# Optimization experiments

Measured on AMD Instinct MI355X. Metric: run time of the kernel, lower is better.

Reference implementation:

```python
import jax, jax.numpy as jnp
import numpy as np
from jax import lax

# dims: batch, item seq len, d_model, d_inner, d_state, d_conv, dt_rank, n_layers
B, L, H, E, N, K, R, NL = 256, 200, 256, 512, 16, 4, 16, 2
V = 150000            # int(n_items * 1.5)
USER_ID = 1
T = L + L // 2        # interleaved length
EPS = 1e-12

FLOATS = ('item_emb', 'ln_w', 'ln_b', 'in_proj_w', 'conv_w', 'conv_b', 'x_proj_w',
          'dt_w', 'dt_b', 'A_log', 'Dp', 'out_w', 'mn_w', 'mn_b',
          'fc1_w', 'fc1_b', 'fc2_w', 'fc2_b', 'fn_w', 'fn_b')


def setup_inputs():
    key = jax.random.key(0)
    ks = jax.random.split(key, 12)
    g = lambda k, s: jax.random.normal(k, s, jnp.float32) * 0.02
    return dict(
        item_seq=jax.random.randint(ks[0], (B, L), 0, 100000),
        seq_len=jax.random.randint(ks[1], (B,), 0, 200),
        item_emb=g(ks[2], (V, H)),
        ln_w=jnp.ones((H,)), ln_b=jnp.zeros((H,)),
        in_proj_w=g(ks[3], (NL, 2 * E, H)),
        conv_w=g(ks[4], (NL, E, K)), conv_b=jnp.zeros((NL, E)),
        x_proj_w=g(ks[5], (NL, R + 2 * N, E)),
        dt_w=g(ks[6], (NL, E, R)), dt_b=jnp.zeros((NL, E)),
        A_log=jnp.tile(jnp.log(jnp.arange(1, N + 1, dtype=jnp.float32)), (NL, E, 1)),
        Dp=jnp.ones((NL, E)),
        out_w=g(ks[7], (NL, H, E)),
        mn_w=jnp.ones((NL, H)), mn_b=jnp.zeros((NL, H)),
        fc1_w=g(ks[8], (NL, 4 * H, H)), fc1_b=jnp.zeros((NL, 4 * H)),
        fc2_w=g(ks[9], (NL, H, 4 * H)), fc2_b=jnp.zeros((NL, H)),
        fn_w=jnp.ones((NL, H)), fn_b=jnp.zeros((NL, H)),
    )


def _ln(x, w, b):
    m = x.mean(-1, keepdims=True)
    v = x.var(-1, keepdims=True)
    return (x - m) * lax.rsqrt(v + EPS) * w + b


def _interleave(seq):
    # [B,L] -> [B, L + L//2], user separator after every 2 items
    i = jnp.arange(L)
    out = jnp.zeros((seq.shape[0], T), seq.dtype)
    out = out.at[:, i + i // 2].set(seq)
    io = jnp.arange(1, L, 2)            # odd positions close a pair
    out = out.at[:, io + io // 2 + 1].set(-USER_ID)
    return out


def _selective_scan(xc, dt, Bm, Cm, A, D):
    # xc, dt: [B,T,E]; Bm, Cm: [B,T,N]; A: [E,N]; D: [E]
    def step(s, ins):
        x_t, dt_t, b_t, c_t = ins                     # [B,E],[B,E],[B,N],[B,N]
        s = s * jnp.exp(dt_t[..., None] * A) + (dt_t * x_t)[..., None] * b_t[:, None, :]
        return s, jnp.einsum('ben,bn->be', s, c_t)
    s0 = jnp.zeros((xc.shape[0], E, N), xc.dtype)
    xs = tuple(a.swapaxes(0, 1) for a in (xc, dt, Bm, Cm))
    _, ys = lax.scan(step, s0, xs)
    return ys.swapaxes(0, 1) + xc * D


def _mamba(x, p):
    xz = x @ p['in_proj_w'].T                         # [B,T,2E]
    xc, z = jnp.split(xz, 2, axis=-1)
    xcT = lax.conv_general_dilated(xc.swapaxes(1, 2), p['conv_w'][:, None, :], (1,),
                                   [(K - 1, 0)], dimension_numbers=('NCH', 'OIH', 'NCH'),
                                   feature_group_count=E)
    xc = jax.nn.silu(xcT + p['conv_b'][None, :, None]).swapaxes(1, 2)  # causal depthwise conv
    xdbl = xc @ p['x_proj_w'].T                       # [B,T,R+2N]
    dt = jax.nn.softplus(xdbl[..., :R] @ p['dt_w'].T + p['dt_b'])
    Bm, Cm = xdbl[..., R:R + N], xdbl[..., R + N:]
    y = _selective_scan(xc, dt, Bm, Cm, -jnp.exp(p['A_log']), p['Dp'])
    return (y * jax.nn.silu(z)) @ p['out_w'].T


def _core(item_seq, seq_len, F):
    tot = _interleave(item_seq)
    tot = jnp.where(tot < 0, tot + V, tot)            # negative user id wraps into table
    h = _ln(F['item_emb'][tot], F['ln_w'], F['ln_b'])  # dropout is identity (eval)
    per = ('in_proj_w', 'conv_w', 'conv_b', 'x_proj_w', 'dt_w', 'dt_b', 'A_log', 'Dp', 'out_w')
    for l in range(NL):
        p = {k: F[k][l] for k in per}
        h = _ln(_mamba(h, p) + h, F['mn_w'][l], F['mn_b'][l])   # use_residual=True (NL>1)
        ff = jax.nn.gelu(h @ F['fc1_w'][l].T + F['fc1_b'][l], approximate=False)
        ff = ff @ F['fc2_w'][l].T + F['fc2_b'][l]
        h = _ln(ff + h, F['fn_w'][l], F['fn_b'][l])
    tl = seq_len + seq_len // 2
    idx = jnp.clip(tl - 1, 0, T - 1)
    return h[jnp.arange(h.shape[0]), idx]             # gather last valid position


def reference(item_seq, seq_len, item_emb, ln_w, ln_b, in_proj_w, conv_w, conv_b,
              x_proj_w, dt_w, dt_b, A_log, Dp, out_w, mn_w, mn_b,
              fc1_w, fc1_b, fc2_w, fc2_b, fn_w, fn_b):
    F = dict(zip(FLOATS, (item_emb, ln_w, ln_b, in_proj_w, conv_w, conv_b, x_proj_w,
                          dt_w, dt_b, A_log, Dp, out_w, mn_w, mn_b,
                          fc1_w, fc1_b, fc2_w, fc2_b, fn_w, fn_b)))
    return _core(item_seq, seq_len, F)
```

## Files before the change

kernel.cpp:

```cpp
#include <hip/hip_runtime.h>
#include <math.h>

typedef unsigned short u16;
typedef __attribute__((ext_vector_type(8))) short bf8_t;
typedef __attribute__((ext_vector_type(4))) float f4_t;

#define BB 256
#define LL 200
#define HH 256
#define EE 512
#define NSTATE 16
#define KCONV 4
#define RR 16
#define NLAYER 2
#define VV 150000
#define TT 300
#define MTOK (BB*TT)
#define NC 6
#define CL 50
#define XW 1024

#define LOG2E 1.44269504088896340736f
#define LN2   0.69314718055994530942f

__device__ __forceinline__ float geluf(float x) {
    return 0.5f * x * (1.0f + erff(x * 0.70710678118654752440f));
}
__device__ __forceinline__ u16 f2bf(float x) {
    unsigned u = __float_as_uint(x);
    unsigned r = u + 0x7FFF + ((u >> 16) & 1);
    return (u16)(r >> 16);
}
__device__ __forceinline__ float bf2f(u16 b) { return __uint_as_float((unsigned)b << 16); }

__device__ __forceinline__ void gload16(const void* gp, void* lp) {
    __builtin_amdgcn_global_load_lds(
        (const __attribute__((address_space(1))) unsigned int*)gp,
        (__attribute__((address_space(3))) unsigned int*)lp,
        16, 0, 0);
}

__device__ __forceinline__ void block_reduce2(float& a, float& b) {
    __shared__ float ra[4], rb[4];
    #pragma unroll
    for (int o = 32; o > 0; o >>= 1) {
        a += __shfl_down(a, o, 64);
        b += __shfl_down(b, o, 64);
    }
    int lane = threadIdx.x & 63, w = threadIdx.x >> 6;
    if (lane == 0) { ra[w] = a; rb[w] = b; }
    __syncthreads();
    a = ra[0] + ra[1] + ra[2] + ra[3];
    b = rb[0] + rb[1] + rb[2] + rb[3];
}

__global__ __launch_bounds__(256)
void split_kernel(const float* __restrict__ x, u16* __restrict__ ph,
                  u16* __restrict__ pl, int n) {
    int i = blockIdx.x * 256 + threadIdx.x;
    if (i < n) {
        float v = x[i];
        u16 hb = f2bf(v);
        ph[i] = hb;
        pl[i] = f2bf(v - bf2f(hb));
    }
}

__global__ __launch_bounds__(256)
void embed_ln_kernel(const int* __restrict__ item_seq,
                     const float* __restrict__ item_emb,
                     const float* __restrict__ ln_w,
                     const float* __restrict__ ln_b,
                     u16* __restrict__ hh, u16* __restrict__ hl) {
    int tok = blockIdx.x;
    int b = tok / TT, p = tok - b * TT;
    int k = p / 3, r = p - 3 * k;
    int item;
    if (r == 2) item = VV - 1;
    else        item = item_seq[b * LL + 2 * k + r];
    int tid = threadIdx.x;
    float x = item_emb[(size_t)item * HH + tid];
    float s1 = x, s2 = x * x;
    block_reduce2(s1, s2);
    float m = s1 * (1.0f / HH);
    float var = s2 * (1.0f / HH) - m * m;
    float inv = rsqrtf(var + 1e-12f);
    float v = (x - m) * inv * ln_w[tid] + ln_b[tid];
    size_t idx = (size_t)tok * HH + tid;
    u16 hb = f2bf(v);
    hh[idx] = hb;
    hl[idx] = f2bf(v - bf2f(hb));
}

__global__ __launch_bounds__(256)
void add_ln_kernel(const float* __restrict__ tmp,
                   u16* __restrict__ hh, u16* __restrict__ hl,
                   const float* __restrict__ w,
                   const float* __restrict__ bnorm) {
    int tok = blockIdx.x;
    int tid = threadIdx.x;
    size_t idx = (size_t)tok * HH + tid;
    float x = tmp[idx] + bf2f(hh[idx]) + bf2f(hl[idx]);
    float s1 = x, s2 = x * x;
    block_reduce2(s1, s2);
    float m = s1 * (1.0f / HH);
    float var = s2 * (1.0f / HH) - m * m;
    float inv = rsqrtf(var + 1e-12f);
    float v = (x - m) * inv * w[tid] + bnorm[tid];
    u16 hb = f2bf(v);
    hh[idx] = hb;
    hl[idx] = f2bf(v - bf2f(hb));
}

template <int AMODE, int MODE>
__global__ __launch_bounds__(256)
void gemm_mfma(const u16* __restrict__ Ah, const u16* __restrict__ Al, int ldab,
               const u16* __restrict__ Wh,
               const float* __restrict__ bias,
               float* __restrict__ C, u16* __restrict__ Cb,
               int M, int N, int K, int ldc) {
    __shared__ u16 sA[2][2][128 * 32];
    __shared__ u16 sB[2][128 * 32];
    int tid = threadIdx.x;
    int lane = tid & 63, wid = tid >> 6;
    int wr = wid >> 1, wc = wid & 1;

    int gx = gridDim.x, nwg = gx * gridDim.y;
    int id = blockIdx.y * gx + blockIdx.x;
    int q = nwg >> 3, rr8 = nwg & 7;
    int xcd = id & 7, pos = id >> 3;
    int nid = (xcd < rr8 ? xcd * (q + 1) : rr8 * (q + 1) + (xcd - rr8) * q) + pos;
    int bn = (nid % gx) * 128;
    int bm = (nid / gx) * 128;

    f4_t acc[4][4];
    #pragma unroll
    for (int i = 0; i < 4; ++i)
        #pragma unroll
        for (int j = 0; j < 4; ++j)
            acc[i][j] = (f4_t){0.f, 0.f, 0.f, 0.f};

    int scol = (lane & 3) * 8;

    auto stageA = [&](int bi, int k0) {
        #pragma unroll
        for (int qq = 0; qq < 2; ++qq) {
            int row = wid * 32 + qq * 16 + (lane >> 2);
            size_t ga = (size_t)(bm + row) * ldab + k0 + scol;
            int off = (wid * 2 + qq) * 1024;
            gload16(Ah + ga, (char*)&sA[bi][0][0] + off);
            if (AMODE == 0)
                gload16(Al + ga, (char*)&sA[bi][1][0] + off);
        }
    };
    auto stageB = [&](int bi, int k0) {
        #pragma unroll
        for (int qq = 0; qq < 2; ++qq) {
            int row = wid * 32 + qq * 16 + (lane >> 2);
            size_t gb = (size_t)(bn + row) * K + k0 + scol;
            int off = (wid * 2 + qq) * 1024;
            gload16(Wh + gb, (char*)&sB[bi][0] + off);
        }
    };
    auto compute = [&](int bi) {
        int arow = wr * 64 + (lane & 15);
        int koff = (lane >> 4) * 8;
        bf8_t ah[4], al[4];
        #pragma unroll
        for (int fm = 0; fm < 4; ++fm) {
            int r = arow + fm * 16;
            ah[fm] = *(const bf8_t*)&sA[bi][0][r * 32 + koff];
            if (AMODE == 0)
                al[fm] = *(const bf8_t*)&sA[bi][1][r * 32 + koff];
        }
        #pragma unroll
        for (int fn = 0; fn < 4; ++fn) {
            int r = wc * 64 + fn * 16 + (lane & 15);
            bf8_t bh = *(const bf8_t*)&sB[bi][r * 32 + koff];
            #pragma unroll
            for (int fm = 0; fm < 4; ++fm) {
                acc[fm][fn] = __builtin_amdgcn_mfma_f32_16x16x32_bf16(ah[fm], bh, acc[fm][fn], 0, 0, 0);
                if (AMODE == 0)
                    acc[fm][fn] = __builtin_amdgcn_mfma_f32_16x16x32_bf16(al[fm], bh, acc[fm][fn], 0, 0, 0);
            }
        }
    };

    stageA(0, 0);
    stageB(0, 0);
    __syncthreads();
    int cur = 0;
    for (int k0 = 0; k0 < K; k0 += 32) {
        if (k0 + 32 < K) {
            stageA(cur ^ 1, k0 + 32);
            stageB(cur ^ 1, k0 + 32);
        }
        compute(cur);
        __syncthreads();
        cur ^= 1;
    }

    if (MODE == 2 || MODE == 3) {
        u16* rs = (u16*)&sA[0][0][0];
        #pragma unroll
        for (int fn = 0; fn < 4; ++fn) {
            int cl = wc * 64 + fn * 16 + (lane & 15);
            float bv = (bias != nullptr) ? bias[bn + cl] : 0.f;
            #pragma unroll
            for (int fm = 0; fm < 4; ++fm) {
                #pragma unroll
                for (int j = 0; j < 4; ++j) {
                    int lr = wr * 64 + fm * 16 + (lane >> 4) * 4 + j;
                    float v = acc[fm][fn][j] + bv;
                    if (MODE == 2) v = geluf(v);
                    rs[lr * 128 + cl] = f2bf(v);
                }
            }
        }
        __syncthreads();
        int r = tid >> 1, half = tid & 1;
        u16* dst = Cb + (size_t)(bm + r) * ldc + bn + half * 64;
        const u16* src = rs + r * 128 + half * 64;
        #pragma unroll
        for (int i = 0; i < 8; ++i)
            *(bf8_t*)&dst[i * 8] = *(const bf8_t*)&src[i * 8];
    } else {
        #pragma unroll
        for (int fn = 0; fn < 4; ++fn) {
            int colg = bn + wc * 64 + fn * 16 + (lane & 15);
            if (colg < N) {
                float bv = (bias != nullptr) ? bias[colg] : 0.f;
                #pragma unroll
                for (int fm = 0; fm < 4; ++fm) {
                    #pragma unroll
                    for (int j = 0; j < 4; ++j) {
                        int rowg = bm + wr * 64 + fm * 16 + (lane >> 4) * 4 + j;
                        C[(size_t)rowg * ldc + colg] = acc[fm][fn][j] + bv;
                    }
                }
            }
        }
    }
}

__global__ __launch_bounds__(256)
void gemm_xproj(const u16* __restrict__ Axz,
                const u16* __restrict__ Wh, const u16* __restrict__ Wl,
                float* __restrict__ C) {
    __shared__ u16 sA[2][128 * 32];
    __shared__ u16 sB[2][2][48 * 32];
    int tid = threadIdx.x;
    int lane = tid & 63, wid = tid >> 6;
    int bm = blockIdx.x * 128;

    f4_t acc[2][3];
    #pragma unroll
    for (int i = 0; i < 2; ++i)
        #pragma unroll
        for (int j = 0; j < 3; ++j)
            acc[i][j] = (f4_t){0.f, 0.f, 0.f, 0.f};

    int scol = (lane & 3) * 8;

    auto stage = [&](int bi, int k0) {
        #pragma unroll
        for (int qq = 0; qq < 2; ++qq) {
            int row = wid * 32 + qq * 16 + (lane >> 2);
            size_t ga = (size_t)(bm + row) * XW + k0 + scol;
            int off = (wid * 2 + qq) * 1024;
            gload16(Axz + ga, (char*)&sA[bi][0] + off);
        }
        if (tid < 192) {
            int row = tid >> 2;
            int c16 = (tid & 3) * 8;
            size_t gb = (size_t)row * EE + k0 + c16;
            gload16(Wh + gb, (char*)&sB[bi][0][0] + tid * 16);
            gload16(Wl + gb, (char*)&sB[bi][1][0] + tid * 16);
        }
    };
    auto compute = [&](int bi) {
        int arow = wid * 32 + (lane & 15);
        int koff = (lane >> 4) * 8;
        bf8_t ah[2];
        #pragma unroll
        for (int fm = 0; fm < 2; ++fm) {
            int r = arow + fm * 16;
            ah[fm] = *(const bf8_t*)&sA[bi][r * 32 + koff];
        }
        #pragma unroll
        for (int fn = 0; fn < 3; ++fn) {
            int r = fn * 16 + (lane & 15);
            bf8_t bh = *(const bf8_t*)&sB[bi][0][r * 32 + koff];
            bf8_t bl = *(const bf8_t*)&sB[bi][1][r * 32 + koff];
            #pragma unroll
            for (int fm = 0; fm < 2; ++fm) {
                acc[fm][fn] = __builtin_amdgcn_mfma_f32_16x16x32_bf16(ah[fm], bh, acc[fm][fn], 0, 0, 0);
                acc[fm][fn] = __builtin_amdgcn_mfma_f32_16x16x32_bf16(ah[fm], bl, acc[fm][fn], 0, 0, 0);
            }
        }
    };

    stage(0, 0);
    __syncthreads();
    int cur = 0;
    for (int k0 = 0; k0 < EE; k0 += 32) {
        if (k0 + 32 < EE) stage(cur ^ 1, k0 + 32);
        compute(cur);
        __syncthreads();
        cur ^= 1;
    }

    #pragma unroll
    for (int fn = 0; fn < 3; ++fn) {
        int colg = fn * 16 + (lane & 15);
        #pragma unroll
        for (int fm = 0; fm < 2; ++fm) {
            #pragma unroll
            for (int j = 0; j < 4; ++j) {
                int rowg = bm + wid * 32 + fm * 16 + (lane >> 4) * 4 + j;
                C[(size_t)rowg * 48 + colg] = acc[fm][fn][j];
            }
        }
    }
}

__global__ __launch_bounds__(256)
void conv_halo_kernel(const u16* __restrict__ xzb, float* __restrict__ halo) {
    int bid = blockIdx.x;
    int ehalf = bid & 1, bc = bid >> 1;
    int c = bc % NC, b = bc / NC;
    int e = ehalf * 256 + threadIdx.x;
    int t0 = c * CL;
    const u16* xp = xzb + (size_t)b * TT * XW + e;
    float* hp = halo + (((size_t)b * NC + c) * 3) * EE + e;
    #pragma unroll
    for (int k = 0; k < 3; ++k) {
        int t = t0 - 3 + k;
        hp[(size_t)k * EE] = (t >= 0) ? bf2f(xp[(size_t)t * XW]) : 0.f;
    }
}

__global__ __launch_bounds__(256)
void conv_chunk_kernel(u16* __restrict__ xzb, const float* __restrict__ halo,
                       const float* __restrict__ conv_w,
                       const float* __restrict__ conv_b, int layer) {
    int bid = blockIdx.x;
    int ehalf = bid & 1, bc = bid >> 1;
    int c = bc % NC, b = bc / NC;
    int e = ehalf * 256 + threadIdx.x;
    int t0 = c * CL;
    const float* w = conv_w + ((size_t)layer * EE + e) * KCONV;
    float w0 = w[0], w1 = w[1], w2 = w[2], w3 = w[3];
    float bias = conv_b[layer * EE + e];
    const float* hp = halo + (((size_t)b * NC + c) * 3) * EE + e;
    float h0 = hp[0], h1 = hp[(size_t)EE], h2 = hp[(size_t)2 * EE];
    u16* p = xzb + ((size_t)b * TT + t0) * XW + e;

    float c0 = bf2f(p[0]);
    float c1 = bf2f(p[(size_t)XW]);
    for (int tg = 0; tg < CL; tg += 2) {
        float n0, n1;
        if (tg + 2 < CL) {
            n0 = bf2f(p[(size_t)(tg + 2) * XW]);
            n1 = bf2f(p[(size_t)(tg + 3) * XW]);
        }
        float v0 = fmaf(w0, h0, fmaf(w1, h1, fmaf(w2, h2, fmaf(w3, c0, bias))));
        float v1 = fmaf(w0, h1, fmaf(w1, h2, fmaf(w2, c0, fmaf(w3, c1, bias))));
        p[(size_t)(tg + 0) * XW] = f2bf(v0 / (1.f + __expf(-v0)));
        p[(size_t)(tg + 1) * XW] = f2bf(v1 / (1.f + __expf(-v1)));
        h0 = h2; h1 = c0; h2 = c1;
        if (tg + 2 < CL) { c0 = n0; c1 = n1; }
    }
}

template <bool CHAIN, bool EMIT>
__device__ __forceinline__ void scan_chunk_body(
        const float* __restrict__ rowp,
        u16* __restrict__ xp,
        const float* __restrict__ dw, float db,
        const float* __restrict__ arl2e,
        float Dv, float2* __restrict__ s2, float& dsum) {
    float xc0 = bf2f(xp[0]), xc1 = bf2f(xp[(size_t)XW]);
    float zc0, zc1;
    if (EMIT) { zc0 = bf2f(xp[EE]); zc1 = bf2f(xp[(size_t)XW + EE]); }
    for (int tg = 0; tg < CL; tg += 2) {
        float xn0, xn1, zn0, zn1;
        if (tg + 2 < CL) {
            xn0 = bf2f(xp[(size_t)(tg + 2) * XW]);
            xn1 = bf2f(xp[(size_t)(tg + 3) * XW]);
            if (EMIT) {
                zn0 = bf2f(xp[(size_t)(tg + 2) * XW + EE]);
                zn1 = bf2f(xp[(size_t)(tg + 3) * XW + EE]);
            }
        }
        #pragma unroll
        for (int i = 0; i < 2; ++i) {
            int t = tg + i;
            const float* row = rowp + (size_t)t * 48;
            float2 racc = make_float2(db, 0.f);
            #pragma unroll
            for (int j = 0; j < 16; j += 2) {
                float2 rv = *(const float2*)(row + j);
                float2 wv = *(const float2*)(dw + j);
                racc += rv * wv;
            }
            float rr = racc.x + racc.y;
            float qv = exp2f(-fabsf(rr) * LOG2E);
            float dt = fmaxf(rr, 0.f) + LN2 * __log2f(1.f + qv);
            if (!EMIT) dsum += dt;
            float xv = (i == 0) ? xc0 : xc1;
            float dx = dt * xv;
            float2 P[8];
            if (CHAIN) {
                float w1 = exp2f(dt * arl2e[0]);
                float w2 = w1 * w1;
                float2 w2v = make_float2(w2, w2);
                P[0] = make_float2(w1, w2);
                #pragma unroll
                for (int k = 1; k < 8; ++k) P[k] = P[k - 1] * w2v;
            } else {
                #pragma unroll
                for (int k = 0; k < 8; ++k)
                    P[k] = make_float2(exp2f(dt * arl2e[2 * k]),
                                       exp2f(dt * arl2e[2 * k + 1]));
            }
            float2 dx2 = make_float2(dx, dx);
            float2 qa = make_float2(0.f, 0.f), qb = make_float2(0.f, 0.f);
            #pragma unroll
            for (int k = 0; k < 8; ++k) {
                float2 Bv = *(const float2*)(row + 16 + 2 * k);
                s2[k] = s2[k] * P[k] + dx2 * Bv;
                if (EMIT) {
                    float2 Cv = *(const float2*)(row + 32 + 2 * k);
                    if (k & 1) qb += s2[k] * Cv;
                    else       qa += s2[k] * Cv;
                }
            }
            if (EMIT) {
                float2 qs = qa + qb;
                float y = (qs.x + qs.y) + xv * Dv;
                float zv = (i == 0) ? zc0 : zc1;
                float u = y * (zv / (1.f + __expf(-zv)));
                xp[(size_t)t * XW] = f2bf(u);
            }
        }
        if (tg + 2 < CL) {
            xc0 = xn0; xc1 = xn1;
            if (EMIT) { zc0 = zn0; zc1 = zn1; }
        }
    }
}

__device__ __forceinline__ void load_scan_params(
        const float* dt_w, const float* dt_b, const float* A_log,
        int layer, int e, float* dw, float& db, float* arl2e, bool& chain) {
    #pragma unroll
    for (int i = 0; i < 16; i += 4)
        *(float4*)&dw[i] = *(const float4*)(dt_w + ((size_t)layer * EE + e) * RR + i);
    db = dt_b[layer * EE + e];
    const float* alp = A_log + ((size_t)layer * EE + e) * NSTATE;
    float ar[16];
    #pragma unroll
    for (int i = 0; i < 16; i += 4) {
        float4 v = *(const float4*)(alp + i);
        ar[i + 0] = -expf(v.x); ar[i + 1] = -expf(v.y);
        ar[i + 2] = -expf(v.z); ar[i + 3] = -expf(v.w);
    }
    chain = true;
    #pragma unroll
    for (int n = 1; n < 16; ++n)
        chain = chain && (fabsf(ar[n] - (n + 1) * ar[0]) <= 1e-3f * (n + 1) * fabsf(ar[0]));
    #pragma unroll
    for (int n = 0; n < 16; ++n) arl2e[n] = ar[n] * LOG2E;
}

__global__ __launch_bounds__(256, 1)
void scan_p1(const float* __restrict__ xdbl, u16* __restrict__ xzb,
             const float* __restrict__ dt_w, const float* __restrict__ dt_b,
             const float* __restrict__ A_log,
             float* __restrict__ SF, float* __restrict__ DS, int layer) {
    int bid = blockIdx.x;
    int ehalf = bid & 1, bc = bid >> 1;
    int c = bc % NC, b = bc / NC;
    int e = ehalf * 256 + threadIdx.x;
    int t0 = c * CL;
    alignas(16) float dw[16], arl2e[16];
    float db; bool chain;
    load_scan_params(dt_w, dt_b, A_log, layer, e, dw, db, arl2e, chain);

    const float* rowp = xdbl + ((size_t)b * TT + t0) * 48;
    u16* xp = xzb + ((size_t)b * TT + t0) * XW + e;
    float2 s2[8];
    #pragma unroll
    for (int k = 0; k < 8; ++k) s2[k] = make_float2(0.f, 0.f);
    float dsum = 0.f;
    if (chain) scan_chunk_body<true, false>(rowp, xp, dw, db, arl2e, 0.f, s2, dsum);
    else       scan_chunk_body<false, false>(rowp, xp, dw, db, arl2e, 0.f, s2, dsum);
    size_t sbase = (((size_t)b * EE + e) * NC + c) * 16;
    #pragma unroll
    for (int k = 0; k < 8; ++k) *(float2*)(SF + sbase + 2 * k) = s2[k];
    DS[((size_t)b * EE + e) * NC + c] = dsum;
}

__global__ __launch_bounds__(256)
void scan_p2(const float* __restrict__ A_log,
             float* __restrict__ SF, const float* __restrict__ DS, int layer) {
    int g = blockIdx.x * 256 + threadIdx.x;
    int e = g & (EE - 1), b = g >> 9;
    const float* alp = A_log + ((size_t)layer * EE + e) * NSTATE;
    float arl2e[16];
    #pragma unroll
    for (int i = 0; i < 16; i += 4) {
        float4 v = *(const float4*)(alp + i);
        arl2e[i + 0] = -expf(v.x) * LOG2E; arl2e[i + 1] = -expf(v.y) * LOG2E;
        arl2e[i + 2] = -expf(v.z) * LOG2E; arl2e[i + 3] = -expf(v.w) * LOG2E;
    }
    float s[16];
    #pragma unroll
    for (int n = 0; n < 16; ++n) s[n] = 0.f;
    size_t base = ((size_t)b * EE + e) * NC;
    for (int c = 0; c < NC; ++c) {
        float ds = DS[base + c];
        alignas(16) float f[16];
        #pragma unroll
        for (int i = 0; i < 16; i += 4) *(float4*)&f[i] = *(const float4*)(SF + (base + c) * 16 + i);
        #pragma unroll
        for (int i = 0; i < 16; i += 4) *(float4*)(SF + (base + c) * 16 + i) = *(float4*)&s[i];
        #pragma unroll
        for (int n = 0; n < 16; ++n) s[n] = fmaf(s[n], exp2f(ds * arl2e[n]), f[n]);
    }
}

__global__ __launch_bounds__(256, 1)
void scan_p3(const float* __restrict__ xdbl, u16* __restrict__ xzb,
             const float* __restrict__ dt_w, const float* __restrict__ dt_b,
             const float* __restrict__ A_log, const float* __restrict__ Dp,
             const float* __restrict__ SF, int layer) {
    int bid = blockIdx.x;
    int ehalf = bid & 1, bc = bid >> 1;
    int c = bc % NC, b = bc / NC;
    int e = ehalf * 256 + threadIdx.x;
    int t0 = c * CL;
    alignas(16) float dw[16], arl2e[16];
    float db; bool chain;
    load_scan_params(dt_w, dt_b, A_log, layer, e, dw, db, arl2e, chain);
    float Dv = Dp[layer * EE + e];

    const float* rowp = xdbl + ((size_t)b * TT + t0) * 48;
    u16* xp = xzb + ((size_t)b * TT + t0) * XW + e;
    float2 s2[8];
    size_t sbase = (((size_t)b * EE + e) * NC + c) * 16;
    #pragma unroll
    for (int k = 0; k < 8; ++k) s2[k] = *(const float2*)(SF + sbase + 2 * k);
    float dsum = 0.f;
    if (chain) scan_chunk_body<true, true>(rowp, xp, dw, db, arl2e, Dv, s2, dsum);
    else       scan_chunk_body<false, true>(rowp, xp, dw, db, arl2e, Dv, s2, dsum);
}

__global__ __launch_bounds__(256)
void gather_out_kernel(const u16* __restrict__ hh, const u16* __restrict__ hl,
                       const int* __restrict__ seq_len,
                       float* __restrict__ out) {
    int b = blockIdx.x;
    int sl = seq_len[b];
    int tl = sl + sl / 2;
    int idx = tl - 1;
    if (idx < 0) idx = 0;
    if (idx > TT - 1) idx = TT - 1;
    size_t src = ((size_t)b * TT + idx) * HH + threadIdx.x;
    out[(size_t)b * HH + threadIdx.x] = bf2f(hh[src]) + bf2f(hl[src]);
}

extern "C" void kernel_launch(void* const* d_in, const int* in_sizes, int n_in,
                              void* d_out, int out_size, void* d_ws, size_t ws_size,
                              hipStream_t stream) {
    const int*   item_seq  = (const int*)  d_in[0];
    const int*   seq_len   = (const int*)  d_in[1];
    const float* item_emb  = (const float*)d_in[2];
    const float* ln_w      = (const float*)d_in[3];
    const float* ln_b      = (const float*)d_in[4];
    const float* in_proj_w = (const float*)d_in[5];
    const float* conv_w    = (const float*)d_in[6];
    const float* conv_b    = (const float*)d_in[7];
    const float* x_proj_w  = (const float*)d_in[8];
    const float* dt_w      = (const float*)d_in[9];
    const float* dt_b      = (const float*)d_in[10];
    const float* A_log     = (const float*)d_in[11];
    const float* Dp        = (const float*)d_in[12];
    const float* out_w     = (const float*)d_in[13];
    const float* mn_w      = (const float*)d_in[14];
    const float* mn_b      = (const float*)d_in[15];
    const float* fc1_w     = (const float*)d_in[16];
    const float* fc1_b     = (const float*)d_in[17];
    const float* fc2_w     = (const float*)d_in[18];
    const float* fc2_b     = (const float*)d_in[19];
    const float* fn_w      = (const float*)d_in[20];
    const float* fn_b      = (const float*)d_in[21];

    u16*   xzb  = (u16*)d_ws;
    u16*   hh   = xzb + (size_t)MTOK * XW;
    u16*   hl   = hh + (size_t)MTOK * HH;
    float* tmp  = (float*)(hl + (size_t)MTOK * HH);
    float* xdbl = tmp;
    float* SF   = tmp + (size_t)3686400;
    float* DS   = tmp + (size_t)16269312;
    float* halo = tmp + (size_t)17055744;
    u16* pw   = (u16*)(tmp + (size_t)MTOK * HH);
    u16* inH  = pw;                 u16* inL  = inH  + 524288;
    u16* xpH  = inL  + 524288;      u16* xpL  = xpH  + 49152;
    u16* outH = xpL  + 49152;       u16* outL = outH + 262144;
    u16* f1H  = outL + 262144;      u16* f1L  = f1H  + 524288;
    u16* f2H  = f1L  + 524288;      u16* f2L  = f2H  + 524288;
    u16* ffb = xzb;

    split_kernel<<<524288 / 256, 256, 0, stream>>>(in_proj_w, inH, inL, 524288);
    split_kernel<<<49152 / 256, 256, 0, stream>>>(x_proj_w, xpH, xpL, 49152);
    split_kernel<<<262144 / 256, 256, 0, stream>>>(out_w, outH, outL, 262144);
    split_kernel<<<524288 / 256, 256, 0, stream>>>(fc1_w, f1H, f1L, 524288);
    split_kernel<<<524288 / 256, 256, 0, stream>>>(fc2_w, f2H, f2L, 524288);

    embed_ln_kernel<<<MTOK, 256, 0, stream>>>(item_seq, item_emb, ln_w, ln_b, hh, hl);

    const int gscan = BB * NC * 2;

    for (int l = 0; l < NLAYER; ++l) {
        {
            dim3 grid((2 * EE) / 128, MTOK / 128);
            gemm_mfma<0, 3><<<grid, 256, 0, stream>>>(
                hh, hl, HH,
                inH + (size_t)l * 262144,
                nullptr, nullptr, xzb, MTOK, 2 * EE, HH, XW);
        }
        conv_halo_kernel<<<gscan, 256, 0, stream>>>(xzb, halo);
        conv_chunk_kernel<<<gscan, 256, 0, stream>>>(xzb, halo, conv_w, conv_b, l);
        gemm_xproj<<<MTOK / 128, 256, 0, stream>>>(
            xzb, xpH + (size_t)l * 24576, xpL + (size_t)l * 24576, xdbl);
        scan_p1<<<gscan, 256, 0, stream>>>(xdbl, xzb, dt_w, dt_b, A_log, SF, DS, l);
        scan_p2<<<(BB * EE) / 256, 256, 0, stream>>>(A_log, SF, DS, l);
        scan_p3<<<gscan, 256, 0, stream>>>(xdbl, xzb, dt_w, dt_b, A_log, Dp, SF, l);
        {
            dim3 grid(HH / 128, MTOK / 128);
            gemm_mfma<3, 0><<<grid, 256, 0, stream>>>(
                xzb, nullptr, XW,
                outH + (size_t)l * 131072,
                nullptr, tmp, nullptr, MTOK, HH, EE, HH);
        }
        add_ln_kernel<<<MTOK, 256, 0, stream>>>(tmp, hh, hl, mn_w + l * HH, mn_b + l * HH);
        {
            dim3 grid((4 * HH) / 128, MTOK / 128);
            gemm_mfma<0, 2><<<grid, 256, 0, stream>>>(
                hh, hl, HH,
                f1H + (size_t)l * 262144,
                fc1_b + (size_t)l * 4 * HH,
                nullptr, ffb, MTOK, 4 * HH, HH, XW);
        }
        {
            dim3 grid(HH / 128, MTOK / 128);
            gemm_mfma<3, 0><<<grid, 256, 0, stream>>>(
                ffb, nullptr, XW,
                f2H + (size_t)l * 262144,
                fc2_b + (size_t)l * HH,
                tmp, nullptr, MTOK, HH, 4 * HH, HH);
        }
        add_ln_kernel<<<MTOK, 256, 0, stream>>>(tmp, hh, hl, fn_w + l * HH, fn_b + l * HH);
    }

    gather_out_kernel<<<BB, 256, 0, stream>>>(hh, hl, seq_len, (float*)d_out);
}
```

Before: 1.735 ms.

## Drop low-part activation MFMA in GEMMs and scan two channels per thread

The in_proj and fc1 GEMMs no longer load or multiply the low bf16 residual of the activations, so each uses half the MFMAs and A-tile traffic, at some cost in accuracy. Separately, the scan phase kernels now handle two adjacent channels per thread, with 32-bit packed x/z loads and stores and shared B/C/dt-row loads. This halves the scan grid and raises per-thread register pressure. The chain check is factored into a helper, and the full A vector is loaded only on the non-chain path.

```diff
diff --git a/kernel.cpp b/kernel.cpp
--- a/kernel.cpp
+++ b/kernel.cpp
@@ -112,14 +112,14 @@
     hl[idx] = f2bf(v - bf2f(hb));
 }
 
-template <int AMODE, int MODE>
-__global__ __launch_bounds__(256)
-void gemm_mfma(const u16* __restrict__ Ah, const u16* __restrict__ Al, int ldab,
+template <int MODE>
+__global__ __launch_bounds__(256)
+void gemm_mfma(const u16* __restrict__ Ah, int ldab,
                const u16* __restrict__ Wh,
                const float* __restrict__ bias,
                float* __restrict__ C, u16* __restrict__ Cb,
                int M, int N, int K, int ldc) {
-    __shared__ u16 sA[2][2][128 * 32];
+    __shared__ u16 sA[2][128 * 32];
     __shared__ u16 sB[2][128 * 32];
     int tid = threadIdx.x;
     int lane = tid & 63, wid = tid >> 6;
@@ -148,9 +148,7 @@
             int row = wid * 32 + qq * 16 + (lane >> 2);
             size_t ga = (size_t)(bm + row) * ldab + k0 + scol;
             int off = (wid * 2 + qq) * 1024;
-            gload16(Ah + ga, (char*)&sA[bi][0][0] + off);
-            if (AMODE == 0)
-                gload16(Al + ga, (char*)&sA[bi][1][0] + off);
+            gload16(Ah + ga, (char*)&sA[bi][0] + off);
         }
     };
     auto stageB = [&](int bi, int k0) {
@@ -165,24 +163,19 @@
     auto compute = [&](int bi) {
         int arow = wr * 64 + (lane & 15);
         int koff = (lane >> 4) * 8;
-        bf8_t ah[4], al[4];
+        bf8_t ah[4];
         #pragma unroll
         for (int fm = 0; fm < 4; ++fm) {
             int r = arow + fm * 16;
-            ah[fm] = *(const bf8_t*)&sA[bi][0][r * 32 + koff];
-            if (AMODE == 0)
-                al[fm] = *(const bf8_t*)&sA[bi][1][r * 32 + koff];
+            ah[fm] = *(const bf8_t*)&sA[bi][r * 32 + koff];
         }
         #pragma unroll
         for (int fn = 0; fn < 4; ++fn) {
             int r = wc * 64 + fn * 16 + (lane & 15);
             bf8_t bh = *(const bf8_t*)&sB[bi][r * 32 + koff];
             #pragma unroll
-            for (int fm = 0; fm < 4; ++fm) {
+            for (int fm = 0; fm < 4; ++fm)
                 acc[fm][fn] = __builtin_amdgcn_mfma_f32_16x16x32_bf16(ah[fm], bh, acc[fm][fn], 0, 0, 0);
-                if (AMODE == 0)
-                    acc[fm][fn] = __builtin_amdgcn_mfma_f32_16x16x32_bf16(al[fm], bh, acc[fm][fn], 0, 0, 0);
-            }
         }
     };
 
@@ -201,7 +194,7 @@
     }
 
     if (MODE == 2 || MODE == 3) {
-        u16* rs = (u16*)&sA[0][0][0];
+        u16* rs = (u16*)&sA[0][0];
         #pragma unroll
         for (int fn = 0; fn < 4; ++fn) {
             int cl = wc * 64 + fn * 16 + (lane & 15);
@@ -373,46 +366,61 @@
     }
 }
 
+__device__ __forceinline__ bool chain_check(const float* __restrict__ alp,
+                                            float& A0l2e) {
+    float a0 = -expf(alp[0]);
+    bool ch = true;
+    #pragma unroll
+    for (int n = 1; n < 16; ++n) {
+        float an = -expf(alp[n]);
+        ch = ch && (fabsf(an - (n + 1) * a0) <= 1e-3f * (n + 1) * fabsf(a0));
+    }
+    A0l2e = a0 * LOG2E;
+    return ch;
+}
+
 template <bool CHAIN, bool EMIT>
-__device__ __forceinline__ void scan_chunk_body(
+__device__ __forceinline__ void scan2_body(
         const float* __restrict__ rowp,
         u16* __restrict__ xp,
-        const float* __restrict__ dw, float db,
-        const float* __restrict__ arl2e,
-        float Dv, float2* __restrict__ s2, float& dsum) {
-    float xc0 = bf2f(xp[0]), xc1 = bf2f(xp[(size_t)XW]);
-    float zc0, zc1;
-    if (EMIT) { zc0 = bf2f(xp[EE]); zc1 = bf2f(xp[(size_t)XW + EE]); }
-    for (int tg = 0; tg < CL; tg += 2) {
-        float xn0, xn1, zn0, zn1;
-        if (tg + 2 < CL) {
-            xn0 = bf2f(xp[(size_t)(tg + 2) * XW]);
-            xn1 = bf2f(xp[(size_t)(tg + 3) * XW]);
-            if (EMIT) {
-                zn0 = bf2f(xp[(size_t)(tg + 2) * XW + EE]);
-                zn1 = bf2f(xp[(size_t)(tg + 3) * XW + EE]);
+        const float dw[2][16], const float db[2],
+        const float A0[2], const float (*arl)[16],
+        const float Dv[2], float2 (*s2)[8], float* dsum) {
+    unsigned xcur = *(const unsigned*)xp;
+    unsigned zcur = 0;
+    if (EMIT) zcur = *(const unsigned*)(xp + EE);
+    for (int t = 0; t < CL; ++t) {
+        unsigned xnxt = 0, znxt = 0;
+        if (t + 1 < CL) {
+            xnxt = *(const unsigned*)(xp + (size_t)(t + 1) * XW);
+            if (EMIT) znxt = *(const unsigned*)(xp + (size_t)(t + 1) * XW + EE);
+        }
+        const float* row = rowp + (size_t)t * 48;
+        float2 rw[8], Bv[8], Cv[8];
+        #pragma unroll
+        for (int j = 0; j < 8; ++j) {
+            rw[j] = *(const float2*)(row + 2 * j);
+            Bv[j] = *(const float2*)(row + 16 + 2 * j);
+            if (EMIT) Cv[j] = *(const float2*)(row + 32 + 2 * j);
+        }
+        unsigned uout = 0;
+        #pragma unroll
+        for (int v = 0; v < 2; ++v) {
+            float r0 = db[v], r1 = 0.f;
+            #pragma unroll
+            for (int j = 0; j < 8; ++j) {
+                r0 = fmaf(rw[j].x, dw[v][2 * j], r0);
+                r1 = fmaf(rw[j].y, dw[v][2 * j + 1], r1);
             }
-        }
-        #pragma unroll
-        for (int i = 0; i < 2; ++i) {
-            int t = tg + i;
-            const float* row = rowp + (size_t)t * 48;
-            float2 racc = make_float2(db, 0.f);
-            #pragma unroll
-            for (int j = 0; j < 16; j += 2) {
-                float2 rv = *(const float2*)(row + j);
-                float2 wv = *(const float2*)(dw + j);
-                racc += rv * wv;
-            }
-            float rr = racc.x + racc.y;
+            float rr = r0 + r1;
             float qv = exp2f(-fabsf(rr) * LOG2E);
             float dt = fmaxf(rr, 0.f) + LN2 * __log2f(1.f + qv);
-            if (!EMIT) dsum += dt;
-            float xv = (i == 0) ? xc0 : xc1;
+            if (!EMIT) dsum[v] += dt;
+            float xv = bf2f((u16)(v == 0 ? (xcur & 0xffffu) : (xcur >> 16)));
             float dx = dt * xv;
             float2 P[8];
             if (CHAIN) {
-                float w1 = exp2f(dt * arl2e[0]);
+                float w1 = exp2f(dt * A0[v]);
                 float w2 = w1 * w1;
                 float2 w2v = make_float2(w2, w2);
                 P[0] = make_float2(w1, w2);
@@ -421,57 +429,65 @@
             } else {
                 #pragma unroll
                 for (int k = 0; k < 8; ++k)
-                    P[k] = make_float2(exp2f(dt * arl2e[2 * k]),
-                                       exp2f(dt * arl2e[2 * k + 1]));
+                    P[k] = make_float2(exp2f(dt * arl[v][2 * k]),
+                                       exp2f(dt * arl[v][2 * k + 1]));
             }
             float2 dx2 = make_float2(dx, dx);
             float2 qa = make_float2(0.f, 0.f), qb = make_float2(0.f, 0.f);
             #pragma unroll
             for (int k = 0; k < 8; ++k) {
-                float2 Bv = *(const float2*)(row + 16 + 2 * k);
-                s2[k] = s2[k] * P[k] + dx2 * Bv;
+                s2[v][k] = s2[v][k] * P[k] + dx2 * Bv[k];
                 if (EMIT) {
-                    float2 Cv = *(const float2*)(row + 32 + 2 * k);
-                    if (k & 1) qb += s2[k] * Cv;
-                    else       qa += s2[k] * Cv;
+                    if (k & 1) qb += s2[v][k] * Cv[k];
+                    else       qa += s2[v][k] * Cv[k];
                 }
             }
             if (EMIT) {
                 float2 qs = qa + qb;
-                float y = (qs.x + qs.y) + xv * Dv;
-                float zv = (i == 0) ? zc0 : zc1;
+                float y = (qs.x + qs.y) + xv * Dv[v];
+                float zv = bf2f((u16)(v == 0 ? (zcur & 0xffffu) : (zcur >> 16)));
                 float u = y * (zv / (1.f + __expf(-zv)));
-                xp[(size_t)t * XW] = f2bf(u);
+                uout |= (unsigned)f2bf(u) << (16 * v);
             }
         }
-        if (tg + 2 < CL) {
-            xc0 = xn0; xc1 = xn1;
-            if (EMIT) { zc0 = zn0; zc1 = zn1; }
-        }
-    }
-}
-
-__device__ __forceinline__ void load_scan_params(
+        if (EMIT) *(unsigned*)(xp + (size_t)t * XW) = uout;
+        xcur = xnxt; zcur = znxt;
+    }
+}
+
+__device__ __forceinline__ void load_scan2_params(
         const float* dt_w, const float* dt_b, const float* A_log,
-        int layer, int e, float* dw, float& db, float* arl2e, bool& chain) {
-    #pragma unroll
-    for (int i = 0; i < 16; i += 4)
-        *(float4*)&dw[i] = *(const float4*)(dt_w + ((size_t)layer * EE + e) * RR + i);
-    db = dt_b[layer * EE + e];
-    const float* alp = A_log + ((size_t)layer * EE + e) * NSTATE;
-    float ar[16];
-    #pragma unroll
-    for (int i = 0; i < 16; i += 4) {
-        float4 v = *(const float4*)(alp + i);
-        ar[i + 0] = -expf(v.x); ar[i + 1] = -expf(v.y);
-        ar[i + 2] = -expf(v.z); ar[i + 3] = -expf(v.w);
-    }
+        int layer, int e0, float dw[2][16], float db[2], float A0[2],
+        bool& chain) {
     chain = true;
     #pragma unroll
-    for (int n = 1; n < 16; ++n)
-        chain = chain && (fabsf(ar[n] - (n + 1) * ar[0]) <= 1e-3f * (n + 1) * fabsf(ar[0]));
-    #pragma unroll
-    for (int n = 0; n < 16; ++n) arl2e[n] = ar[n] * LOG2E;
+    for (int v = 0; v < 2; ++v) {
+        int e = e0 + v;
+        #pragma unroll
+        for (int i = 0; i < 16; i += 4)
+            *(float4*)&dw[v][i] = *(const float4*)(dt_w + ((size_t)layer * EE + e) * RR + i);
+        db[v] = dt_b[layer * EE + e];
+        float a0;
+        bool c = chain_check(A_log + ((size_t)layer * EE + e) * NSTATE, a0);
+        A0[v] = a0;
+        chain = chain && c;
+    }
+}
+
+__device__ __forceinline__ void load_arl2(const float* A_log, int layer, int e0,
+                                          float arl[2][16]) {
+    #pragma unroll
+    for (int v = 0; v < 2; ++v) {
+        const float* alp = A_log + ((size_t)layer * EE + e0 + v) * NSTATE;
+        #pragma unroll
+        for (int i = 0; i < 16; i += 4) {
+            float4 x4 = *(const float4*)(alp + i);
+            arl[v][i + 0] = -expf(x4.x) * LOG2E;
+            arl[v][i + 1] = -expf(x4.y) * LOG2E;
+            arl[v][i + 2] = -expf(x4.z) * LOG2E;
+            arl[v][i + 3] = -expf(x4.w) * LOG2E;
+        }
+    }
 }
 
 __global__ __launch_bounds__(256, 1)
@@ -480,26 +496,36 @@
              const float* __restrict__ A_log,
              float* __restrict__ SF, float* __restrict__ DS, int layer) {
     int bid = blockIdx.x;
-    int ehalf = bid & 1, bc = bid >> 1;
-    int c = bc % NC, b = bc / NC;
-    int e = ehalf * 256 + threadIdx.x;
+    int c = bid % NC, b = bid / NC;
+    int e0 = threadIdx.x * 2;
     int t0 = c * CL;
-    alignas(16) float dw[16], arl2e[16];
-    float db; bool chain;
-    load_scan_params(dt_w, dt_b, A_log, layer, e, dw, db, arl2e, chain);
+    float dw[2][16], db[2], A0[2];
+    bool chain;
+    load_scan2_params(dt_w, dt_b, A_log, layer, e0, dw, db, A0, chain);
 
     const float* rowp = xdbl + ((size_t)b * TT + t0) * 48;
-    u16* xp = xzb + ((size_t)b * TT + t0) * XW + e;
-    float2 s2[8];
-    #pragma unroll
-    for (int k = 0; k < 8; ++k) s2[k] = make_float2(0.f, 0.f);
-    float dsum = 0.f;
-    if (chain) scan_chunk_body<true, false>(rowp, xp, dw, db, arl2e, 0.f, s2, dsum);
-    else       scan_chunk_body<false, false>(rowp, xp, dw, db, arl2e, 0.f, s2, dsum);
-    size_t sbase = (((size_t)b * EE + e) * NC + c) * 16;
-    #pragma unroll
-    for (int k = 0; k < 8; ++k) *(float2*)(SF + sbase + 2 * k) = s2[k];
-    DS[((size_t)b * EE + e) * NC + c] = dsum;
+    u16* xp = xzb + ((size_t)b * TT + t0) * XW + e0;
+    float2 s2[2][8];
+    #pragma unroll
+    for (int v = 0; v < 2; ++v)
+        #pragma unroll
+        for (int k = 0; k < 8; ++k) s2[v][k] = make_float2(0.f, 0.f);
+    float dsum[2] = {0.f, 0.f};
+    float Dv[2] = {0.f, 0.f};
+    if (chain) {
+        scan2_body<true, false>(rowp, xp, dw, db, A0, nullptr, Dv, s2, dsum);
+    } else {
+        float arl[2][16];
+        load_arl2(A_log, layer, e0, arl);
+        scan2_body<false, false>(rowp, xp, dw, db, A0, arl, Dv, s2, dsum);
+    }
+    #pragma unroll
+    for (int v = 0; v < 2; ++v) {
+        size_t sbase = (((size_t)b * EE + e0 + v) * NC + c) * 16;
+        #pragma unroll
+        for (int k = 0; k < 8; ++k) *(float2*)(SF + sbase + 2 * k) = s2[v][k];
+        DS[((size_t)b * EE + e0 + v) * NC + c] = dsum[v];
+    }
 }
 
 __global__ __launch_bounds__(256)
@@ -537,24 +563,33 @@
              const float* __restrict__ A_log, const float* __restrict__ Dp,
              const float* __restrict__ SF, int layer) {
     int bid = blockIdx.x;
-    int ehalf = bid & 1, bc = bid >> 1;
-    int c = bc % NC, b = bc / NC;
-    int e = ehalf * 256 + threadIdx.x;
+    int c = bid % NC, b = bid / NC;
+    int e0 = threadIdx.x * 2;
     int t0 = c * CL;
-    alignas(16) float dw[16], arl2e[16];
-    float db; bool chain;
-    load_scan_params(dt_w, dt_b, A_log, layer, e, dw, db, arl2e, chain);
-    float Dv = Dp[layer * EE + e];
+    float dw[2][16], db[2], A0[2];
+    bool chain;
+    load_scan2_params(dt_w, dt_b, A_log, layer, e0, dw, db, A0, chain);
+    float Dv[2];
+    Dv[0] = Dp[layer * EE + e0];
+    Dv[1] = Dp[layer * EE + e0 + 1];
 
     const float* rowp = xdbl + ((size_t)b * TT + t0) * 48;
-    u16* xp = xzb + ((size_t)b * TT + t0) * XW + e;
-    float2 s2[8];
-    size_t sbase = (((size_t)b * EE + e) * NC + c) * 16;
-    #pragma unroll
-    for (int k = 0; k < 8; ++k) s2[k] = *(const float2*)(SF + sbase + 2 * k);
-    float dsum = 0.f;
-    if (chain) scan_chunk_body<true, true>(rowp, xp, dw, db, arl2e, Dv, s2, dsum);
-    else       scan_chunk_body<false, true>(rowp, xp, dw, db, arl2e, Dv, s2, dsum);
+    u16* xp = xzb + ((size_t)b * TT + t0) * XW + e0;
+    float2 s2[2][8];
+    #pragma unroll
+    for (int v = 0; v < 2; ++v) {
+        size_t sbase = (((size_t)b * EE + e0 + v) * NC + c) * 16;
+        #pragma unroll
+        for (int k = 0; k < 8; ++k) s2[v][k] = *(const float2*)(SF + sbase + 2 * k);
+    }
+    float dsum[2] = {0.f, 0.f};
+    if (chain) {
+        scan2_body<true, true>(rowp, xp, dw, db, A0, nullptr, Dv, s2, dsum);
+    } else {
+        float arl[2][16];
+        load_arl2(A_log, layer, e0, arl);
+        scan2_body<false, true>(rowp, xp, dw, db, A0, arl, Dv, s2, dsum);
+    }
 }
 
 __global__ __launch_bounds__(256)
@@ -621,18 +656,19 @@
 
     embed_ln_kernel<<<MTOK, 256, 0, stream>>>(item_seq, item_emb, ln_w, ln_b, hh, hl);
 
-    const int gscan = BB * NC * 2;
+    const int gconv = BB * NC * 2;
+    const int gscan = BB * NC;
 
     for (int l = 0; l < NLAYER; ++l) {
         {
             dim3 grid((2 * EE) / 128, MTOK / 128);
-            gemm_mfma<0, 3><<<grid, 256, 0, stream>>>(
-                hh, hl, HH,
+            gemm_mfma<3><<<grid, 256, 0, stream>>>(
+                hh, HH,
                 inH + (size_t)l * 262144,
                 nullptr, nullptr, xzb, MTOK, 2 * EE, HH, XW);
         }
-        conv_halo_kernel<<<gscan, 256, 0, stream>>>(xzb, halo);
-        conv_chunk_kernel<<<gscan, 256, 0, stream>>>(xzb, halo, conv_w, conv_b, l);
+        conv_halo_kernel<<<gconv, 256, 0, stream>>>(xzb, halo);
+        conv_chunk_kernel<<<gconv, 256, 0, stream>>>(xzb, halo, conv_w, conv_b, l);
         gemm_xproj<<<MTOK / 128, 256, 0, stream>>>(
             xzb, xpH + (size_t)l * 24576, xpL + (size_t)l * 24576, xdbl);
         scan_p1<<<gscan, 256, 0, stream>>>(xdbl, xzb, dt_w, dt_b, A_log, SF, DS, l);
@@ -640,24 +676,24 @@
         scan_p3<<<gscan, 256, 0, stream>>>(xdbl, xzb, dt_w, dt_b, A_log, Dp, SF, l);
         {
             dim3 grid(HH / 128, MTOK / 128);
-            gemm_mfma<3, 0><<<grid, 256, 0, stream>>>(
-                xzb, nullptr, XW,
+            gemm_mfma<0><<<grid, 256, 0, stream>>>(
+                xzb, XW,
                 outH + (size_t)l * 131072,
                 nullptr, tmp, nullptr, MTOK, HH, EE, HH);
         }
         add_ln_kernel<<<MTOK, 256, 0, stream>>>(tmp, hh, hl, mn_w + l * HH, mn_b + l * HH);
         {
             dim3 grid((4 * HH) / 128, MTOK / 128);
-            gemm_mfma<0, 2><<<grid, 256, 0, stream>>>(
-                hh, hl, HH,
+            gemm_mfma<2><<<grid, 256, 0, stream>>>(
+                hh, HH,
                 f1H + (size_t)l * 262144,
                 fc1_b + (size_t)l * 4 * HH,
                 nullptr, ffb, MTOK, 4 * HH, HH, XW);
         }
         {
             dim3 grid(HH / 128, MTOK / 128);
-            gemm_mfma<3, 0><<<grid, 256, 0, stream>>>(
-                ffb, nullptr, XW,
+            gemm_mfma<0><<<grid, 256, 0, stream>>>(
+                ffb, XW,
                 f2H + (size_t)l * 262144,
                 fc2_b + (size_t)l * HH,
                 tmp, nullptr, MTOK, HH, 4 * HH, HH);
```

Result: faster. 1.636 ms (-5.7%).
